# Performance work log

Measured on AMD Instinct MI355X. Metric: run time of the kernel, lower is better.

## Reference

```python
import jax, jax.numpy as jnp
import numpy as np

B, S, HID = 2, 2048, 1024
NH = 16
HD = HID // NH  # 64
ROPE_BASE = 10000.0


def _rope_cos_sin(seq_len, head_dim, dtype):
    inv_freq = 1.0 / (ROPE_BASE ** (jnp.arange(0, head_dim, 2, dtype=jnp.float32) / head_dim))
    t = jnp.arange(seq_len, dtype=jnp.float32)
    freqs = jnp.einsum('s,d->sd', t, inv_freq)            # [S, HD/2]
    emb = jnp.concatenate([freqs, freqs], axis=-1)        # [S, HD]
    return jnp.cos(emb).astype(dtype), jnp.sin(emb).astype(dtype)


def _rotate_half(x):
    x1, x2 = jnp.split(x, 2, axis=-1)
    return jnp.concatenate([-x2, x1], axis=-1)


def setup_inputs() -> dict:
    key = jax.random.key(0)
    k1, k2, k3, k4 = jax.random.split(key, 4)
    hidden_states = jax.random.normal(k1, (B, S, HID), dtype=jnp.float32)
    scale_in = 1.0 / np.sqrt(HID)
    w_qkv = jax.random.normal(k2, (HID, 3 * HID), dtype=jnp.float32) * scale_in
    w_dense = jax.random.normal(k3, (HID, HID), dtype=jnp.float32) * scale_in
    b_dense = jax.random.normal(k4, (HID,), dtype=jnp.float32) * 0.01
    return {"hidden_states": hidden_states, "w_qkv": w_qkv,
            "w_dense": w_dense, "b_dense": b_dense}


def reference(hidden_states, w_qkv, w_dense, b_dense):
    b, s, _ = hidden_states.shape
    # Fused QKV projection (no bias), split into q, k, v of [B, S, HID] each.
    fused = hidden_states @ w_qkv                           # [B, S, 3*HID]
    q, k, v = jnp.split(fused, 3, axis=-1)
    # [B, S, NH, HD] -> [B, NH, S, HD]
    q = q.reshape(b, s, NH, HD).transpose(0, 2, 1, 3)
    k = k.reshape(b, s, NH, HD).transpose(0, 2, 1, 3)
    v = v.reshape(b, s, NH, HD).transpose(0, 2, 1, 3)
    # Rotary position embedding on q and k.
    cos, sin = _rope_cos_sin(s, HD, hidden_states.dtype)    # [S, HD]
    cos = cos[None, None, :, :]
    sin = sin[None, None, :, :]
    q = q * cos + _rotate_half(q) * sin
    k = k * cos + _rotate_half(k) * sin
    # Naive causal attention with full score materialization.
    inv_norm = 1.0 / jnp.sqrt(jnp.asarray(HD, dtype=hidden_states.dtype))
    scores = jnp.einsum('bhqd,bhkd->bhqk', q, k) * inv_norm  # [B, NH, S, S]
    causal = jnp.tril(jnp.ones((s, s), dtype=bool))[None, None, :, :]
    neg = jnp.asarray(jnp.finfo(scores.dtype).min, dtype=scores.dtype)
    scores = jnp.where(causal, scores, neg)
    attn = jax.nn.softmax(scores, axis=-1)
    out = jnp.einsum('bhqk,bhkd->bhqd', attn, v)            # [B, NH, S, HD]
    out = out.transpose(0, 2, 1, 3).reshape(b, s, HID)
    return out @ w_dense + b_dense
```

## Files before the change

### kernel.cpp

```cpp
#include <hip/hip_runtime.h>

#define B_ 2
#define S_ 2048
#define HID_ 1024
#define NH_ 16
#define HD_ 64

typedef _Float16 half8 __attribute__((ext_vector_type(8)));
typedef float f32x4 __attribute__((ext_vector_type(4)));

__device__ __forceinline__ void gload16(const _Float16* g, _Float16* l) {
    __builtin_amdgcn_global_load_lds(
        (const __attribute__((address_space(1))) void*)g,
        (__attribute__((address_space(3))) void*)l, 16, 0, 0);
}


__device__ __forceinline__ void tr32(const float* __restrict__ in, _Float16* __restrict__ out,
                                     int K, int N, int n0, int k0, int tx, int ty,
                                     float (*tile)[33]) {
    #pragma unroll
    for (int i2 = 0; i2 < 32; i2 += 8)
        tile[ty + i2][tx] = in[(size_t)(k0 + ty + i2) * N + n0 + tx];
    __syncthreads();
    #pragma unroll
    for (int i2 = 0; i2 < 32; i2 += 8)
        out[(size_t)(n0 + ty + i2) * K + k0 + tx] = (_Float16)tile[tx][ty + i2];
}

__global__ __launch_bounds__(256) void k_prep(
        const float* __restrict__ hidden, const float* __restrict__ w_qkv,
        const float* __restrict__ w_dense, _Float16* __restrict__ hh,
        _Float16* __restrict__ wqkvT, _Float16* __restrict__ wdT,
        float* __restrict__ cos_t, float* __restrict__ sin_t) {
    int b = blockIdx.x, t = threadIdx.x;
    __shared__ float tile[32][33];
    if (b < 2048) {
        int i = (b * 256 + t) * 8;
        float4 a = *(const float4*)&hidden[i];
        float4 c = *(const float4*)&hidden[i + 4];
        half8 h;
        h[0] = (_Float16)a.x; h[1] = (_Float16)a.y; h[2] = (_Float16)a.z; h[3] = (_Float16)a.w;
        h[4] = (_Float16)c.x; h[5] = (_Float16)c.y; h[6] = (_Float16)c.z; h[7] = (_Float16)c.w;
        *(half8*)&hh[i] = h;
    } else if (b < 5120) {
        int bb = b - 2048;
        tr32(w_qkv, wqkvT, HID_, 3 * HID_, (bb % 96) * 32, (bb / 96) * 32, t & 31, t >> 5, tile);
    } else if (b < 6144) {
        int bb = b - 5120;
        tr32(w_dense, wdT, HID_, HID_, (bb % 32) * 32, (bb / 32) * 32, t & 31, t >> 5, tile);
    } else {
        int bb = b - 6144;
        int s = bb * 8 + (t >> 5);
        int ii = t & 31;
        float inv = powf(10000.0f, -(float)(2 * ii) / 64.0f);
        float ang = (float)s * inv;
        cos_t[s * 32 + ii] = cosf(ang);
        sin_t[s * 32 + ii] = sinf(ang);
    }
}

__global__ __launch_bounds__(256) void k_reshape_rope(
        const _Float16* __restrict__ fused, const float* __restrict__ cos_t,
        const float* __restrict__ sin_t, _Float16* __restrict__ qh,
        _Float16* __restrict__ kh, _Float16* __restrict__ vt) {
    int blk = blockIdx.x;
    int s0 = (blk & 31) * 64;
    int bh = blk >> 5;
    int h = bh & 15;
    int t = threadIdx.x;
    int r = t >> 2, dq0 = (t & 3) * 16;
    int s = s0 + r;
    const _Float16* fr = fused + ((size_t)(bh >> 4) * S_ + s) * 3072;
    size_t qkbase = ((size_t)bh * S_ + s) * HD_;
    int pq0 = dq0 ^ 32;
    float sgn = (dq0 < 32) ? -1.f : 1.f;

    half8 qm[2], qp[2], km[2], kp[2], vm[2];
    qm[0] = *(const half8*)&fr[h * 64 + dq0];
    qm[1] = *(const half8*)&fr[h * 64 + dq0 + 8];
    qp[0] = *(const half8*)&fr[h * 64 + pq0];
    qp[1] = *(const half8*)&fr[h * 64 + pq0 + 8];
    km[0] = *(const half8*)&fr[1024 + h * 64 + dq0];
    km[1] = *(const half8*)&fr[1024 + h * 64 + dq0 + 8];
    kp[0] = *(const half8*)&fr[1024 + h * 64 + pq0];
    kp[1] = *(const half8*)&fr[1024 + h * 64 + pq0 + 8];
    vm[0] = *(const half8*)&fr[2048 + h * 64 + dq0];
    vm[1] = *(const half8*)&fr[2048 + h * 64 + dq0 + 8];

    const float* cb = &cos_t[s * 32 + (dq0 & 31)];
    const float* sb = &sin_t[s * 32 + (dq0 & 31)];
    half8 qo[2], ko[2];
    #pragma unroll
    for (int v8 = 0; v8 < 2; ++v8)
        #pragma unroll
        for (int j = 0; j < 8; ++j) {
            float cs = cb[v8 * 8 + j], sn = sb[v8 * 8 + j];
            qo[v8][j] = (_Float16)((float)qm[v8][j] * cs + sgn * (float)qp[v8][j] * sn);
            ko[v8][j] = (_Float16)((float)km[v8][j] * cs + sgn * (float)kp[v8][j] * sn);
        }
    *(half8*)&qh[qkbase + dq0]     = qo[0];
    *(half8*)&qh[qkbase + dq0 + 8] = qo[1];
    *(half8*)&kh[qkbase + dq0]     = ko[0];
    *(half8*)&kh[qkbase + dq0 + 8] = ko[1];

    __shared__ _Float16 vtile[64][80];
    *(half8*)&vtile[r][dq0]     = vm[0];
    *(half8*)&vtile[r][dq0 + 8] = vm[1];
    __syncthreads();
    int dd = t >> 2, sc0 = (t & 3) * 16;
    _Float16 vv[16];
    #pragma unroll
    for (int j = 0; j < 16; ++j)
        vv[j] = vtile[sc0 + j][dd];
    size_t vbase = ((size_t)bh * HD_ + dd) * (size_t)S_ + s0 + sc0;
    *(half8*)&vt[vbase]     = *(half8*)&vv[0];
    *(half8*)&vt[vbase + 8] = *(half8*)&vv[8];
}

template <bool WRITE_F32>
__global__ __launch_bounds__(256) void k_gemm(const _Float16* __restrict__ A,
                                              const _Float16* __restrict__ Bt,
                                              void* __restrict__ Cout,
                                              const float* __restrict__ bias,
                                              int M, int N, int K) {
    __shared__ _Float16 At[2][128 * 32];
    __shared__ _Float16 Bts[2][128 * 32];
    int t = threadIdx.x;
    int nb = N >> 7;
    int nwg = (M >> 7) * nb;
    int bid = blockIdx.x;
    int swz = (bid & 7) * (nwg >> 3) + (bid >> 3);
    int m0 = (swz / nb) << 7;
    int n0 = (swz % nb) << 7;
    int lane = t & 63, wid = t >> 6;
    int wm = (wid >> 1) * 64, wn = (wid & 1) * 64;
    int lr = lane & 15, lg = lane >> 4;

    int srow = t >> 2, sc = (t & 3) * 8;
    const _Float16* Ap  = &A[(size_t)(m0 + srow) * K + sc];
    const _Float16* Ap2 = &A[(size_t)(m0 + 64 + srow) * K + sc];
    const _Float16* Bp  = &Bt[(size_t)(n0 + srow) * K + sc];
    const _Float16* Bp2 = &Bt[(size_t)(n0 + 64 + srow) * K + sc];

    auto STAGE = [&](int bsel, int k0) {
        gload16(Ap + k0,  &At[bsel][t * 8]);
        gload16(Ap2 + k0, &At[bsel][(256 + t) * 8]);
        gload16(Bp + k0,  &Bts[bsel][t * 8]);
        gload16(Bp2 + k0, &Bts[bsel][(256 + t) * 8]);
    };

    f32x4 acc[4][4] = {};
    STAGE(0, 0);
    int nk = K >> 5;
    for (int ti = 0; ti < nk; ++ti) {
        int cur = ti & 1;
        __syncthreads();
        if (ti + 1 < nk) STAGE(cur ^ 1, (ti + 1) << 5);
        half8 af[4], bf[4];
        #pragma unroll
        for (int i = 0; i < 4; ++i)
            af[i] = *(const half8*)&At[cur][(wm + i * 16 + lr) * 32 + lg * 8];
        #pragma unroll
        for (int i = 0; i < 4; ++i)
            bf[i] = *(const half8*)&Bts[cur][(wn + i * 16 + lr) * 32 + lg * 8];
        __builtin_amdgcn_s_setprio(1);
        #pragma unroll
        for (int i = 0; i < 4; ++i)
            #pragma unroll
            for (int j = 0; j < 4; ++j)
                acc[i][j] = __builtin_amdgcn_mfma_f32_16x16x32_f16(af[i], bf[j], acc[i][j], 0, 0, 0);
        __builtin_amdgcn_s_setprio(0);
        __syncthreads();
    }
    #pragma unroll
    for (int i = 0; i < 4; ++i) {
        #pragma unroll
        for (int j = 0; j < 4; ++j) {
            #pragma unroll
            for (int r2 = 0; r2 < 4; ++r2) {
                int row = m0 + wm + i * 16 + lg * 4 + r2;
                int col = n0 + wn + j * 16 + lr;
                float v = acc[i][j][r2];
                if constexpr (WRITE_F32)
                    ((float*)Cout)[(size_t)row * N + col] = v + bias[col];
                else
                    ((_Float16*)Cout)[(size_t)row * N + col] = (_Float16)v;
            }
        }
    }
}

__global__ __launch_bounds__(256) void k_attn(const _Float16* __restrict__ qh,
                                              const _Float16* __restrict__ kh,
                                              const _Float16* __restrict__ vt,
                                              _Float16* __restrict__ attn_out) {
    int blk0 = blockIdx.x;
    int x = blk0 & 7;
    int i = blk0 >> 3;
    int bh = x * 4 + (i >> 4);
    int p = i & 15;
    int qtA = p, qtB = 31 - p;
    int t = threadIdx.x, lane = t & 63, w = t >> 6;
    int lr = lane & 15, lg = lane >> 4;
    const _Float16* Qb = qh + (size_t)bh * S_ * HD_;
    const _Float16* Kb = kh + (size_t)bh * S_ * HD_;
    const _Float16* Vb = vt + (size_t)bh * HD_ * S_;

    __shared__ _Float16 Kt[2][64 * 64];
    __shared__ _Float16 Vt[2][64 * 64];
    __shared__ _Float16 PlB[4][16 * 64];
    __shared__ _Float16 PlA[4][16 * 64];

    const _Float16 qsc = (_Float16)0.18033688f;
    half8 qfA[2], qfB[2];
    {
        int qA = qtA * 64 + w * 16 + lr;
        int qB = qtB * 64 + w * 16 + lr;
        #pragma unroll
        for (int dh = 0; dh < 2; ++dh) {
            qfA[dh] = *(const half8*)&Qb[(size_t)qA * 64 + dh * 32 + lg * 8];
            qfB[dh] = *(const half8*)&Qb[(size_t)qB * 64 + dh * 32 + lg * 8];
            #pragma unroll
            for (int j = 0; j < 8; ++j) { qfA[dh][j] *= qsc; qfB[dh][j] *= qsc; }
        }
    }

    f32x4 accA[4] = {}, accB[4] = {};
    float mA = -1e30f, lA = 0.f, mB = -1e30f, lB = 0.f;
    int swq = lr & 7;
    int s0 = 0, cur = 0;

    auto STAGE = [&](int bsel, int s0s) {
        #pragma unroll
        for (int cc = 0; cc < 2; ++cc) {
            int base = w * 128 + cc * 64;
            int idx = base + lane;
            int row = idx >> 3;
            int cg = (idx & 7) ^ (row & 7);
            gload16(&Kb[(size_t)(s0s + row) * 64 + cg * 8], &Kt[bsel][base * 8]);
            gload16(&Vb[(size_t)row * S_ + s0s + cg * 8], &Vt[bsel][base * 8]);
        }
    };

    auto smax = [&](f32x4 (&z)[4], float& mrun, float& lrun, f32x4 (&acc)[4],
                    _Float16* plw, bool domask, int q0g, half8 (&pa)[2]) {
        int qw0 = q0g + w * 16;
        if (domask) {
            int q = qw0 + lr;
            #pragma unroll
            for (int nt = 0; nt < 4; ++nt)
                #pragma unroll
                for (int r = 0; r < 4; ++r) {
                    int kv = s0 + nt * 16 + lg * 4 + r;
                    if (kv > q) z[nt][r] = -1e30f;
                }
        }
        float mx = z[0][0];
        #pragma unroll
        for (int nt = 0; nt < 4; ++nt)
            #pragma unroll
            for (int r = 0; r < 4; ++r) mx = fmaxf(mx, z[nt][r]);
        mx = fmaxf(mx, __shfl_xor(mx, 16));
        mx = fmaxf(mx, __shfl_xor(mx, 32));

        if (!__all(mx <= mrun + 11.f)) {
            float mnew = fmaxf(mrun, mx);
            float fac = __builtin_amdgcn_exp2f(mrun - mnew);
            mrun = mnew;
            lrun *= fac;
            float facv[4];
            #pragma unroll
            for (int r = 0; r < 4; ++r) facv[r] = __shfl(fac, lg * 4 + r);
            #pragma unroll
            for (int dt = 0; dt < 4; ++dt)
                #pragma unroll
                for (int r = 0; r < 4; ++r) acc[dt][r] *= facv[r];
        }

        float rs = 0.f;
        #pragma unroll
        for (int nt = 0; nt < 4; ++nt)
            #pragma unroll
            for (int r = 0; r < 4; ++r) {
                float pv = __builtin_amdgcn_exp2f(z[nt][r] - mrun);
                z[nt][r] = pv;
                rs += pv;
            }
        rs += __shfl_xor(rs, 16);
        rs += __shfl_xor(rs, 32);
        lrun += rs;

        #pragma unroll
        for (int nt = 0; nt < 4; ++nt) {
            unsigned ua = __builtin_bit_cast(unsigned, __builtin_amdgcn_cvt_pkrtz(z[nt][0], z[nt][1]));
            unsigned ub = __builtin_bit_cast(unsigned, __builtin_amdgcn_cvt_pkrtz(z[nt][2], z[nt][3]));
            int chunk = 2 * nt + (lg >> 1);
            char* pp = (char*)plw + lr * 128 + ((chunk ^ swq) * 16) + (lg & 1) * 8;
            *(uint2*)pp = make_uint2(ua, ub);
        }
        #pragma unroll
        for (int hh = 0; hh < 2; ++hh)
            pa[hh] = *(const half8*)((const char*)plw + lr * 128 + (((4 * hh + lg) ^ swq) * 16));
    };

    STAGE(0, 0);
    for (int ti = 0; ti <= qtB; ++ti) {
        s0 = ti << 6;
        cur = ti & 1;
        __syncthreads();
        if (ti < qtB) STAGE(cur ^ 1, s0 + 64);

        if (ti <= qtA) {
            f32x4 zB[4], zA[4];
            __builtin_amdgcn_s_setprio(1);
            #pragma unroll
            for (int nt = 0; nt < 4; ++nt) {
                int rr = nt * 16 + lr;
                half8 kf0 = *(const half8*)&Kt[cur][rr * 64 + ((lg ^ swq) * 8)];
                half8 kf1 = *(const half8*)&Kt[cur][rr * 64 + (((4 + lg) ^ swq) * 8)];
                f32x4 z = {0.f, 0.f, 0.f, 0.f};
                z = __builtin_amdgcn_mfma_f32_16x16x32_f16(kf0, qfB[0], z, 0, 0, 0);
                z = __builtin_amdgcn_mfma_f32_16x16x32_f16(kf1, qfB[1], z, 0, 0, 0);
                zB[nt] = z;
                f32x4 y = {0.f, 0.f, 0.f, 0.f};
                y = __builtin_amdgcn_mfma_f32_16x16x32_f16(kf0, qfA[0], y, 0, 0, 0);
                y = __builtin_amdgcn_mfma_f32_16x16x32_f16(kf1, qfA[1], y, 0, 0, 0);
                zA[nt] = y;
            }
            __builtin_amdgcn_s_setprio(0);
            half8 paB[2], paA[2];
            smax(zB, mB, lB, accB, &PlB[w][0], false, qtB * 64, paB);
            smax(zA, mA, lA, accA, &PlA[w][0], ti == qtA, qtA * 64, paA);
            __builtin_amdgcn_s_setprio(1);
            #pragma unroll
            for (int dt = 0; dt < 4; ++dt) {
                int vr = dt * 16 + lr;
                #pragma unroll
                for (int hh = 0; hh < 2; ++hh) {
                    half8 vb = *(const half8*)&Vt[cur][vr * 64 + (((4 * hh + lg) ^ swq) * 8)];
                    accB[dt] = __builtin_amdgcn_mfma_f32_16x16x32_f16(paB[hh], vb, accB[dt], 0, 0, 0);
                    accA[dt] = __builtin_amdgcn_mfma_f32_16x16x32_f16(paA[hh], vb, accA[dt], 0, 0, 0);
                }
            }
            __builtin_amdgcn_s_setprio(0);
        } else {
            f32x4 zB[4];
            __builtin_amdgcn_s_setprio(1);
            #pragma unroll
            for (int nt = 0; nt < 4; ++nt) {
                int rr = nt * 16 + lr;
                half8 kf0 = *(const half8*)&Kt[cur][rr * 64 + ((lg ^ swq) * 8)];
                half8 kf1 = *(const half8*)&Kt[cur][rr * 64 + (((4 + lg) ^ swq) * 8)];
                f32x4 z = {0.f, 0.f, 0.f, 0.f};
                z = __builtin_amdgcn_mfma_f32_16x16x32_f16(kf0, qfB[0], z, 0, 0, 0);
                z = __builtin_amdgcn_mfma_f32_16x16x32_f16(kf1, qfB[1], z, 0, 0, 0);
                zB[nt] = z;
            }
            __builtin_amdgcn_s_setprio(0);
            half8 paB[2];
            smax(zB, mB, lB, accB, &PlB[w][0], ti == qtB, qtB * 64, paB);
            __builtin_amdgcn_s_setprio(1);
            #pragma unroll
            for (int dt = 0; dt < 4; ++dt) {
                int vr = dt * 16 + lr;
                #pragma unroll
                for (int hh = 0; hh < 2; ++hh) {
                    half8 vb = *(const half8*)&Vt[cur][vr * 64 + (((4 * hh + lg) ^ swq) * 8)];
                    accB[dt] = __builtin_amdgcn_mfma_f32_16x16x32_f16(paB[hh], vb, accB[dt], 0, 0, 0);
                }
            }
            __builtin_amdgcn_s_setprio(0);
        }
    }

    int b = bh >> 4, h = bh & 15;
    auto writeout = [&](const f32x4* acc, float lrun, int q0g) {
        float linv[4];
        #pragma unroll
        for (int r = 0; r < 4; ++r) linv[r] = 1.0f / __shfl(lrun, lg * 4 + r);
        #pragma unroll
        for (int dt = 0; dt < 4; ++dt)
            #pragma unroll
            for (int r = 0; r < 4; ++r) {
                int s = q0g + w * 16 + lg * 4 + r;
                attn_out[((size_t)b * S_ + s) * HID_ + h * 64 + dt * 16 + lr] =
                    (_Float16)(acc[dt][r] * linv[r]);
            }
    };
    writeout(accB, lB, qtB * 64);
    writeout(accA, lA, qtA * 64);
}


extern "C" void kernel_launch(void* const* d_in, const int* in_sizes, int n_in,
                              void* d_out, int out_size, void* d_ws, size_t ws_size,
                              hipStream_t stream) {
    const float* hidden  = (const float*)d_in[0];
    const float* w_qkv   = (const float*)d_in[1];
    const float* w_dense = (const float*)d_in[2];
    const float* b_dense = (const float*)d_in[3];
    float* out = (float*)d_out;
    char* ws = (char*)d_ws;

    _Float16* hh     = (_Float16*)(ws + 0);
    _Float16* wqkvT  = (_Float16*)(ws + 8388608);
    _Float16* wdT    = (_Float16*)(ws + 14680064);
    float*    cos_t  = (float*)   (ws + 16777216);
    float*    sin_t  = (float*)   (ws + 17039360);
    _Float16* fused  = (_Float16*)(ws + 17301504);
    _Float16* kh     = (_Float16*)(ws + 42467328);
    _Float16* vt     = (_Float16*)(ws + 50855936);
    _Float16* qh     = hh;
    _Float16* attn_o = fused;

    k_prep<<<6400, 256, 0, stream>>>(hidden, w_qkv, w_dense, hh, wqkvT, wdT, cos_t, sin_t);

    k_gemm<false><<<(B_ * S_ / 128) * (3 * HID_ / 128), 256, 0, stream>>>(
        hh, wqkvT, (void*)fused, nullptr, B_ * S_, 3 * HID_, HID_);

    k_reshape_rope<<<B_ * NH_ * (S_ / 64), 256, 0, stream>>>(fused, cos_t, sin_t, qh, kh, vt);

    k_attn<<<B_ * NH_ * (S_ / 64) / 2, 256, 0, stream>>>(qh, kh, vt, attn_o);

    k_gemm<true><<<(B_ * S_ / 128) * (HID_ / 128), 256, 0, stream>>>(
        attn_o, wdT, (void*)out, b_dense, B_ * S_, HID_, HID_);
}
```

Before: 200.2 us.

## Fuse RoPE and head reshape/V transpose into QKV GEMM epilogue

Removes the separate reshape+RoPE kernel by applying rotary embedding and writing head-major Q/K directly from the QKV GEMM accumulators, with the rotate-half partner taken from the same thread's accumulator tile. V tiles are staged through shared memory in the epilogue and written transposed. This drops the fused fp16 intermediate round trip through HBM and one launch. In exchange the GEMM epilogue does scattered 2-byte stores and extra cos/sin loads, and the workspace layout changes.

```diff
diff --git a/kernel.cpp b/kernel.cpp
--- a/kernel.cpp
+++ b/kernel.cpp
@@ -60,72 +60,20 @@
     }
 }
 
-__global__ __launch_bounds__(256) void k_reshape_rope(
-        const _Float16* __restrict__ fused, const float* __restrict__ cos_t,
-        const float* __restrict__ sin_t, _Float16* __restrict__ qh,
-        _Float16* __restrict__ kh, _Float16* __restrict__ vt) {
-    int blk = blockIdx.x;
-    int s0 = (blk & 31) * 64;
-    int bh = blk >> 5;
-    int h = bh & 15;
-    int t = threadIdx.x;
-    int r = t >> 2, dq0 = (t & 3) * 16;
-    int s = s0 + r;
-    const _Float16* fr = fused + ((size_t)(bh >> 4) * S_ + s) * 3072;
-    size_t qkbase = ((size_t)bh * S_ + s) * HD_;
-    int pq0 = dq0 ^ 32;
-    float sgn = (dq0 < 32) ? -1.f : 1.f;
-
-    half8 qm[2], qp[2], km[2], kp[2], vm[2];
-    qm[0] = *(const half8*)&fr[h * 64 + dq0];
-    qm[1] = *(const half8*)&fr[h * 64 + dq0 + 8];
-    qp[0] = *(const half8*)&fr[h * 64 + pq0];
-    qp[1] = *(const half8*)&fr[h * 64 + pq0 + 8];
-    km[0] = *(const half8*)&fr[1024 + h * 64 + dq0];
-    km[1] = *(const half8*)&fr[1024 + h * 64 + dq0 + 8];
-    kp[0] = *(const half8*)&fr[1024 + h * 64 + pq0];
-    kp[1] = *(const half8*)&fr[1024 + h * 64 + pq0 + 8];
-    vm[0] = *(const half8*)&fr[2048 + h * 64 + dq0];
-    vm[1] = *(const half8*)&fr[2048 + h * 64 + dq0 + 8];
-
-    const float* cb = &cos_t[s * 32 + (dq0 & 31)];
-    const float* sb = &sin_t[s * 32 + (dq0 & 31)];
-    half8 qo[2], ko[2];
-    #pragma unroll
-    for (int v8 = 0; v8 < 2; ++v8)
-        #pragma unroll
-        for (int j = 0; j < 8; ++j) {
-            float cs = cb[v8 * 8 + j], sn = sb[v8 * 8 + j];
-            qo[v8][j] = (_Float16)((float)qm[v8][j] * cs + sgn * (float)qp[v8][j] * sn);
-            ko[v8][j] = (_Float16)((float)km[v8][j] * cs + sgn * (float)kp[v8][j] * sn);
-        }
-    *(half8*)&qh[qkbase + dq0]     = qo[0];
-    *(half8*)&qh[qkbase + dq0 + 8] = qo[1];
-    *(half8*)&kh[qkbase + dq0]     = ko[0];
-    *(half8*)&kh[qkbase + dq0 + 8] = ko[1];
-
-    __shared__ _Float16 vtile[64][80];
-    *(half8*)&vtile[r][dq0]     = vm[0];
-    *(half8*)&vtile[r][dq0 + 8] = vm[1];
-    __syncthreads();
-    int dd = t >> 2, sc0 = (t & 3) * 16;
-    _Float16 vv[16];
-    #pragma unroll
-    for (int j = 0; j < 16; ++j)
-        vv[j] = vtile[sc0 + j][dd];
-    size_t vbase = ((size_t)bh * HD_ + dd) * (size_t)S_ + s0 + sc0;
-    *(half8*)&vt[vbase]     = *(half8*)&vv[0];
-    *(half8*)&vt[vbase + 8] = *(half8*)&vv[8];
-}
-
-template <bool WRITE_F32>
+template <bool WRITE_F32, bool QKV_EP>
 __global__ __launch_bounds__(256) void k_gemm(const _Float16* __restrict__ A,
                                               const _Float16* __restrict__ Bt,
                                               void* __restrict__ Cout,
                                               const float* __restrict__ bias,
-                                              int M, int N, int K) {
-    __shared__ _Float16 At[2][128 * 32];
-    __shared__ _Float16 Bts[2][128 * 32];
+                                              int M, int N, int K,
+                                              const float* __restrict__ cos_t,
+                                              const float* __restrict__ sin_t,
+                                              _Float16* __restrict__ qh,
+                                              _Float16* __restrict__ kh,
+                                              _Float16* __restrict__ vt) {
+    __shared__ _Float16 smem[16640];
+    _Float16* At  = smem;
+    _Float16* Bts = smem + 8192;
     int t = threadIdx.x;
     int nb = N >> 7;
     int nwg = (M >> 7) * nb;
@@ -144,10 +92,10 @@
     const _Float16* Bp2 = &Bt[(size_t)(n0 + 64 + srow) * K + sc];
 
     auto STAGE = [&](int bsel, int k0) {
-        gload16(Ap + k0,  &At[bsel][t * 8]);
-        gload16(Ap2 + k0, &At[bsel][(256 + t) * 8]);
-        gload16(Bp + k0,  &Bts[bsel][t * 8]);
-        gload16(Bp2 + k0, &Bts[bsel][(256 + t) * 8]);
+        gload16(Ap + k0,  &At[bsel * 4096 + t * 8]);
+        gload16(Ap2 + k0, &At[bsel * 4096 + (256 + t) * 8]);
+        gload16(Bp + k0,  &Bts[bsel * 4096 + t * 8]);
+        gload16(Bp2 + k0, &Bts[bsel * 4096 + (256 + t) * 8]);
     };
 
     f32x4 acc[4][4] = {};
@@ -160,10 +108,10 @@
         half8 af[4], bf[4];
         #pragma unroll
         for (int i = 0; i < 4; ++i)
-            af[i] = *(const half8*)&At[cur][(wm + i * 16 + lr) * 32 + lg * 8];
+            af[i] = *(const half8*)&At[cur * 4096 + (wm + i * 16 + lr) * 32 + lg * 8];
         #pragma unroll
         for (int i = 0; i < 4; ++i)
-            bf[i] = *(const half8*)&Bts[cur][(wn + i * 16 + lr) * 32 + lg * 8];
+            bf[i] = *(const half8*)&Bts[cur * 4096 + (wn + i * 16 + lr) * 32 + lg * 8];
         __builtin_amdgcn_s_setprio(1);
         #pragma unroll
         for (int i = 0; i < 4; ++i)
@@ -173,21 +121,80 @@
         __builtin_amdgcn_s_setprio(0);
         __syncthreads();
     }
-    #pragma unroll
-    for (int i = 0; i < 4; ++i) {
-        #pragma unroll
-        for (int j = 0; j < 4; ++j) {
-            #pragma unroll
-            for (int r2 = 0; r2 < 4; ++r2) {
-                int row = m0 + wm + i * 16 + lg * 4 + r2;
-                int col = n0 + wn + j * 16 + lr;
-                float v = acc[i][j][r2];
-                if constexpr (WRITE_F32)
-                    ((float*)Cout)[(size_t)row * N + col] = v + bias[col];
-                else
-                    ((_Float16*)Cout)[(size_t)row * N + col] = (_Float16)v;
-            }
-        }
+
+    if constexpr (QKV_EP) {
+        int sect = n0 >> 10;
+        int h0 = (n0 & 1023) >> 6;
+        int h = h0 + (wn >> 6);
+        if (sect < 2) {
+            _Float16* dst = (sect == 0) ? qh : kh;
+            #pragma unroll
+            for (int i = 0; i < 4; ++i) {
+                int rowb = m0 + wm + i * 16 + lg * 4;
+                #pragma unroll
+                for (int r = 0; r < 4; ++r) {
+                    int row = rowb + r;
+                    int s = row & (S_ - 1);
+                    int b2 = row >> 11;
+                    float cs0 = cos_t[s * 32 + lr];
+                    float sn0 = sin_t[s * 32 + lr];
+                    float cs1 = cos_t[s * 32 + 16 + lr];
+                    float sn1 = sin_t[s * 32 + 16 + lr];
+                    size_t base = (((size_t)b2 * NH_ + h) * S_ + s) * HD_;
+                    #pragma unroll
+                    for (int j = 0; j < 4; ++j) {
+                        int d = j * 16 + lr;
+                        float v = acc[i][j][r];
+                        float pv = acc[i][j ^ 2][r];
+                        float cs = (j & 1) ? cs1 : cs0;
+                        float sn = (j & 1) ? sn1 : sn0;
+                        float res = v * cs + ((j < 2) ? -pv : pv) * sn;
+                        dst[base + d] = (_Float16)res;
+                    }
+                }
+            }
+        } else {
+            _Float16 (*vts)[130] = (_Float16(*)[130])smem;
+            #pragma unroll
+            for (int i = 0; i < 4; ++i)
+                #pragma unroll
+                for (int j = 0; j < 4; ++j)
+                    #pragma unroll
+                    for (int r = 0; r < 4; ++r)
+                        vts[wm + i * 16 + lg * 4 + r][wn + j * 16 + lr] = (_Float16)acc[i][j][r];
+            __syncthreads();
+            int b2 = m0 >> 11;
+            int sbase = m0 & (S_ - 1);
+            int dd = t >> 2, sc0 = (t & 3) * 16;
+            #pragma unroll
+            for (int hs = 0; hs < 2; ++hs)
+                #pragma unroll
+                for (int dh = 0; dh < 2; ++dh) {
+                    _Float16 tmp[16];
+                    #pragma unroll
+                    for (int jj = 0; jj < 16; ++jj)
+                        tmp[jj] = vts[hs * 64 + sc0 + jj][dh * 64 + dd];
+                    size_t vrow = (((size_t)b2 * NH_ + h0 + dh) * HD_ + dd) * S_
+                                  + sbase + hs * 64 + sc0;
+                    *(half8*)&vt[vrow]     = *(half8*)&tmp[0];
+                    *(half8*)&vt[vrow + 8] = *(half8*)&tmp[8];
+                }
+        }
+    } else {
+        #pragma unroll
+        for (int i = 0; i < 4; ++i)
+            #pragma unroll
+            for (int j = 0; j < 4; ++j)
+                #pragma unroll
+                for (int r2 = 0; r2 < 4; ++r2) {
+                    int row = m0 + wm + i * 16 + lg * 4 + r2;
+                    int col = n0 + wn + j * 16 + lr;
+                    float v = acc[i][j][r2];
+                    if constexpr (WRITE_F32)
+                        ((float*)Cout)[(size_t)row * N + col] = v + bias[col];
+                    else
+                        ((_Float16*)Cout)[(size_t)row * N + col] = (_Float16)v;
+                }
     }
 }
 
@@ -408,21 +415,19 @@
     _Float16* wdT    = (_Float16*)(ws + 14680064);
     float*    cos_t  = (float*)   (ws + 16777216);
     float*    sin_t  = (float*)   (ws + 17039360);
-    _Float16* fused  = (_Float16*)(ws + 17301504);
-    _Float16* kh     = (_Float16*)(ws + 42467328);
-    _Float16* vt     = (_Float16*)(ws + 50855936);
-    _Float16* qh     = hh;
-    _Float16* attn_o = fused;
+    _Float16* qh     = (_Float16*)(ws + 17301504);
+    _Float16* kh     = (_Float16*)(ws + 25690112);
+    _Float16* vt     = (_Float16*)(ws + 34078720);
+    _Float16* attn_o = hh;
 
     k_prep<<<6400, 256, 0, stream>>>(hidden, w_qkv, w_dense, hh, wqkvT, wdT, cos_t, sin_t);
 
-    k_gemm<false><<<(B_ * S_ / 128) * (3 * HID_ / 128), 256, 0, stream>>>(
-        hh, wqkvT, (void*)fused, nullptr, B_ * S_, 3 * HID_, HID_);
-
-    k_reshape_rope<<<B_ * NH_ * (S_ / 64), 256, 0, stream>>>(fused, cos_t, sin_t, qh, kh, vt);
+    k_gemm<false, true><<<(B_ * S_ / 128) * (3 * HID_ / 128), 256, 0, stream>>>(
+        hh, wqkvT, nullptr, nullptr, B_ * S_, 3 * HID_, HID_, cos_t, sin_t, qh, kh, vt);
 
     k_attn<<<B_ * NH_ * (S_ / 64) / 2, 256, 0, stream>>>(qh, kh, vt, attn_o);
 
-    k_gemm<true><<<(B_ * S_ / 128) * (HID_ / 128), 256, 0, stream>>>(
-        attn_o, wdT, (void*)out, b_dense, B_ * S_, HID_, HID_);
-}
+    k_gemm<true, false><<<(B_ * S_ / 128) * (HID_ / 128), 256, 0, stream>>>(
+        attn_o, wdT, (void*)out, b_dense, B_ * S_, HID_, HID_,
+        nullptr, nullptr, nullptr, nullptr, nullptr);
+}
```

New measurement: 194.3 us. 2.9% less time.
